# Optimization experiments

Measured on AMD Instinct MI355X. Metric: run time of the kernel, lower is better.

Reference implementation:

```python
import jax, jax.numpy as jnp
import numpy as np

B, H, N, L = 8, 128, 64, 8192
LOG_DT_MIN, LOG_DT_MAX = float(np.log(0.001)), float(np.log(0.1))


def setup_inputs() -> dict:
    key = jax.random.key(0)
    k_x, k_are, k_aim, k_c, k_dt = jax.random.split(key, 5)
    x = jax.random.normal(k_x, (B, H, L), dtype=jnp.float32)
    # A_re: negative real parts (clipped to <= -1e-4 in forward anyway)
    A_re = -jax.random.uniform(k_are, (H, N, 1), dtype=jnp.float32, minval=0.1, maxval=1.0)
    A_im = jax.random.normal(k_aim, (H, N, 1), dtype=jnp.float32) * float(np.pi)
    C = (0.5 ** 0.5) * jax.random.normal(k_c, (H, N, 2), dtype=jnp.float32)
    D = jnp.ones((1, H, 1), dtype=jnp.float32)
    u = jax.random.uniform(k_dt, (H, 1, 1), dtype=jnp.float32)
    log_delta = u * (LOG_DT_MAX - LOG_DT_MIN) + LOG_DT_MIN
    return {"x": x, "A_re": A_re, "A_im": A_im, "C": C, "D": D, "log_delta": log_delta}


def reference(x, A_re, A_im, C, D, log_delta):
    seq_len = x.shape[-1]
    # ---- S4D-ZOH kernel generation ----
    A = jnp.minimum(A_re, -1e-4) + 1j * A_im            # (H, N, 1) complex
    Cc = C[..., 0:1] + 1j * C[..., 1:2]                 # (H, N, 1) complex
    step = jnp.exp(log_delta)                           # (H, 1, 1)
    dA = step * A                                       # (H, N, 1)
    times = jnp.arange(seq_len, dtype=jnp.float32)[None, None, :]  # (1, 1, L)
    part = jnp.exp(times * dA)                          # (H, N, L)
    cons = (jnp.exp(dA) - 1.0) / A                      # (H, N, 1)
    K = jnp.sum(Cc * cons * part, axis=-2).real         # (H, L)
    # ---- causal conv via FFT (torch pads both to length 2L) ----
    n = seq_len + K.shape[-1]                           # 2L
    xd = jnp.fft.rfft(x, n=n, axis=-1)                  # (B, H, L+1)
    Kd = jnp.fft.rfft(K[None], n=n, axis=-1)            # (1, H, L+1)
    conv = jnp.fft.irfft(xd * Kd, n=n, axis=-1)[:, :, :seq_len]
    return conv + D * x
```

## Files before the change

kernel.cpp:

```cpp
#include <hip/hip_runtime.h>
#include <hip/hip_bf16.h>
#include <math.h>

#define B_ 8
#define H_ 128
#define N_ 64
#define L_ 8192
#define MCH 64
#define SCH (L_ / MCH)
#define EROW 136

typedef __attribute__((ext_vector_type(8))) short bf16x8;
typedef __attribute__((ext_vector_type(4))) float f32x4;

__device__ __forceinline__ float bf2f(ushort s) { return __uint_as_float(((uint)s) << 16); }
__device__ __forceinline__ uint packbf2(float a, float b) {
    __hip_bfloat162 h = __float22bfloat162_rn(make_float2(a, b));
    union { __hip_bfloat162 h2; uint u; } cv; cv.h2 = h;
    return cv.u;
}
__device__ __forceinline__ bf16x8 pack_bf8(float4 a, float4 b) {
    union { uint u[4]; bf16x8 v; } r;
    r.u[0] = packbf2(a.x, a.y); r.u[1] = packbf2(a.z, a.w);
    r.u[2] = packbf2(b.x, b.y); r.u[3] = packbf2(b.z, b.w);
    return r.v;
}

__global__ __launch_bounds__(256) void s4d_build(
    const float* __restrict__ A_re, const float* __restrict__ A_im,
    const float* __restrict__ C, const float* __restrict__ D,
    const float* __restrict__ log_delta,
    ushort* __restrict__ wsT, ushort* __restrict__ wsP,
    ushort* __restrict__ wsQ, float2* __restrict__ wsRM)
{
    __shared__ float kpart[64][65];
    __shared__ float kv[64];
    __shared__ uint  pbuf[64 * 68];

    const int h = blockIdx.x;
    const int tid = threadIdx.x;
    const int n = tid & 63;
    const int g = tid >> 6;

    float are = fminf(A_re[h * N_ + n], -1e-4f);
    float aim = A_im[h * N_ + n];
    float step = expf(log_delta[h]);
    float dre = step * are, dim = step * aim;
    float er = expf(dre);
    float sd, cd; sincosf(dim, &sd, &cd);
    float rr = er * cd;
    float ri = er * sd;
    float cre = C[(h * N_ + n) * 2 + 0];
    float cim = C[(h * N_ + n) * 2 + 1];
    float inv  = 1.0f / (are * are + aim * aim);
    float numr = rr - 1.0f, numi = ri;
    float consr = (numr * are + numi * aim) * inv;
    float consi = (numi * are - numr * aim) * inv;
    float wr = cre * consr - cim * consi;
    float wi = cre * consi + cim * consr;
    float dval = D[h];

    auto rp = [&](float d, float& pr, float& pi) {
        float e = __expf(d * dre);
        float ang = d * dim;
        float s = __sinf(ang), c2 = __cosf(ang);
        pr = e * c2; pi = e * s;
    };

#pragma unroll
    for (int j = 0; j < 16; ++j) {
        int d = g * 16 + j;
        float pr, pi; rp((float)d, pr, pi);
        kpart[d][n] = wr * pr - wi * pi;
    }
    __syncthreads();
    if (tid < 64) {
        float s = 0.f;
#pragma unroll
        for (int m = 0; m < 64; ++m) s += kpart[tid][m];
        kv[tid] = s;
    }
    __syncthreads();

    {
        uint tw[8];
#pragma unroll
        for (int i = 0; i < 8; ++i) {
            int t0 = g * 16 + 2 * i, t1 = t0 + 1;
            float v0 = (t0 <= n) ? kv[n - t0] : 0.f;
            float v1 = (t1 <= n) ? kv[n - t1] : 0.f;
            if (t0 == n) v0 += dval;
            if (t1 == n) v1 += dval;
            tw[i] = packbf2(v0, v1);
        }
        uint4* dT = (uint4*)(wsT + ((size_t)h * 64 + n) * 64 + g * 16);
        dT[0] = ((uint4*)tw)[0]; dT[1] = ((uint4*)tw)[1];
    }

    {
        uint qr[8], qi[8];
#pragma unroll
        for (int i = 0; i < 8; ++i) {
            int t0 = g * 16 + 2 * i;
            float ar0, ai0, ar1, ai1;
            rp((float)(63 - t0), ar0, ai0);
            rp((float)(62 - t0), ar1, ai1);
            qr[i] = packbf2(ar0, ar1);
            qi[i] = packbf2(ai0, ai1);
        }
        uint4* dQ0 = (uint4*)(wsQ + ((size_t)h * 128 + 2 * n    ) * 64 + g * 16);
        uint4* dQ1 = (uint4*)(wsQ + ((size_t)h * 128 + 2 * n + 1) * 64 + g * 16);
        dQ0[0] = ((uint4*)qr)[0]; dQ0[1] = ((uint4*)qr)[1];
        dQ1[0] = ((uint4*)qi)[0]; dQ1[1] = ((uint4*)qi)[1];
    }

#pragma unroll
    for (int i = 0; i < 16; ++i) {
        int j = g * 16 + i;
        float pr, pi; rp((float)(j + 1), pr, pi);
        float ur = wr * pr - wi * pi;
        float ui = wr * pi + wi * pr;
        pbuf[j * 68 + n] = packbf2(ur, -ui);
    }
    if (tid < 64) {
        float mr = rr, mi = ri;
#pragma unroll
        for (int k = 0; k < 6; ++k) { float tr = mr*mr - mi*mi, ti = 2.f*mr*mi; mr = tr; mi = ti; }
        wsRM[h * 64 + n] = make_float2(mr, mi);
    }
    __syncthreads();
    {
        uint4* dP = (uint4*)(wsP + ((size_t)h * 64 + n) * 128 + g * 32);
        const uint* src = &pbuf[n * 68 + g * 16];
        dP[0] = *(const uint4*)(src);
        dP[1] = *(const uint4*)(src + 4);
        dP[2] = *(const uint4*)(src + 8);
        dP[3] = *(const uint4*)(src + 12);
    }
}

__global__ __launch_bounds__(256, 4) void s4d_main(
    const float* __restrict__ x,
    const ushort* __restrict__ wsT, const ushort* __restrict__ wsP,
    const ushort* __restrict__ wsQ, const float2* __restrict__ wsRM,
    float* __restrict__ out)
{
    __shared__ ushort EBUF[SCH * EROW];
    __shared__ float segr[4][64], segi[4][64];

    const int seq = blockIdx.x;
    const int h   = seq % H_;
    const int tid = threadIdx.x;
    const int w   = tid >> 6;
    const int lane = tid & 63;
    const int n16 = lane & 15, q = lane >> 4;

    const float* xs = x + (size_t)seq * L_;

    bf16x8 xb[2][2];
#pragma unroll
    for (int ic = 0; ic < 2; ++ic) {
        int c = (2 * w + ic) * 16 + n16;
#pragma unroll
        for (int kc = 0; kc < 2; ++kc) {
            const float* p = xs + c * MCH + kc * 32 + q * 8;
            float4 f0 = *(const float4*)p;
            float4 f1 = *(const float4*)(p + 4);
            xb[ic][kc] = pack_bf8(f0, f1);
        }
    }

    const ushort* Qh = wsQ + (size_t)h * 128 * 64;
#pragma unroll
    for (int rt = 0; rt < 8; ++rt) {
        bf16x8 a0 = *(const bf16x8*)(Qh + ((size_t)(rt * 16 + n16)) * 64 +      q * 8);
        bf16x8 a1 = *(const bf16x8*)(Qh + ((size_t)(rt * 16 + n16)) * 64 + 32 + q * 8);
#pragma unroll
        for (int ic = 0; ic < 2; ++ic) {
            f32x4 acc = {0.f, 0.f, 0.f, 0.f};
            acc = __builtin_amdgcn_mfma_f32_16x16x32_bf16(a0, xb[ic][0], acc, 0, 0, 0);
            acc = __builtin_amdgcn_mfma_f32_16x16x32_bf16(a1, xb[ic][1], acc, 0, 0, 0);
            int c = (2 * w + ic) * 16 + n16;
            uint2 st = make_uint2(packbf2(acc[0], acc[1]), packbf2(acc[2], acc[3]));
            *(uint2*)&EBUF[c * EROW + rt * 16 + q * 4] = st;
        }
    }
    __syncthreads();

    {
        const int nB = tid & 63, gB = tid >> 6;
        float2 rm = wsRM[h * 64 + nB];
        float mr = rm.x, mi = rm.y;
        float m32r = mr, m32i = mi;
#pragma unroll
        for (int k = 0; k < 5; ++k) {
            float tr = m32r * m32r - m32i * m32i, ti = 2.f * m32r * m32i;
            m32r = tr; m32i = ti;
        }
        float sr = 0.f, si = 0.f;
#pragma unroll
        for (int j = 0; j < 32; ++j) {
            uint e = *(const uint*)&EBUF[(gB * 32 + j) * EROW + 2 * nB];
            float er2 = bf2f((ushort)(e & 0xffffu)), ei2 = bf2f((ushort)(e >> 16));
            float nr = er2 + mr * sr - mi * si;
            float ni = ei2 + mr * si + mi * sr;
            sr = nr; si = ni;
        }
        segr[gB][nB] = sr; segi[gB][nB] = si;
        __syncthreads();
        float pr2 = 0.f, pi2 = 0.f;
        for (int gp = 0; gp < gB; ++gp) {
            float Er = segr[gp][nB], Ei = segi[gp][nB];
            float nr = Er + m32r * pr2 - m32i * pi2;
            float ni = Ei + m32r * pi2 + m32i * pr2;
            pr2 = nr; pi2 = ni;
        }
        sr = pr2; si = pi2;
#pragma unroll
        for (int j = 0; j < 32; ++j) {
            uint* ep = (uint*)&EBUF[(gB * 32 + j) * EROW + 2 * nB];
            uint e = *ep;
            float er2 = bf2f((ushort)(e & 0xffffu)), ei2 = bf2f((ushort)(e >> 16));
            *ep = packbf2(sr, si);
            float nr = er2 + mr * sr - mi * si;
            float ni = ei2 + mr * si + mi * sr;
            sr = nr; si = ni;
        }
    }
    __syncthreads();

    const ushort* Th = wsT + (size_t)h * 64 * 64;
    const ushort* Ph = wsP + (size_t)h * 64 * 128;
    float* op = out + (size_t)seq * L_;
#pragma unroll
    for (int rt = 0; rt < 4; ++rt) {
        bf16x8 t0 = *(const bf16x8*)(Th + ((size_t)(rt * 16 + n16)) * 64 +      q * 8);
        bf16x8 t1 = *(const bf16x8*)(Th + ((size_t)(rt * 16 + n16)) * 64 + 32 + q * 8);
        bf16x8 p0 = *(const bf16x8*)(Ph + ((size_t)(rt * 16 + n16)) * 128 +       q * 8);
        bf16x8 p1 = *(const bf16x8*)(Ph + ((size_t)(rt * 16 + n16)) * 128 +  32 + q * 8);
        bf16x8 p2 = *(const bf16x8*)(Ph + ((size_t)(rt * 16 + n16)) * 128 +  64 + q * 8);
        bf16x8 p3 = *(const bf16x8*)(Ph + ((size_t)(rt * 16 + n16)) * 128 +  96 + q * 8);
#pragma unroll
        for (int ic = 0; ic < 2; ++ic) {
            int c = (2 * w + ic) * 16 + n16;
            f32x4 accT = {0.f, 0.f, 0.f, 0.f};
            f32x4 accP = {0.f, 0.f, 0.f, 0.f};
            accT = __builtin_amdgcn_mfma_f32_16x16x32_bf16(t0, xb[ic][0], accT, 0, 0, 0);
            accP = __builtin_amdgcn_mfma_f32_16x16x32_bf16(p0,
                       *(const bf16x8*)&EBUF[c * EROW +       q * 8], accP, 0, 0, 0);
            accT = __builtin_amdgcn_mfma_f32_16x16x32_bf16(t1, xb[ic][1], accT, 0, 0, 0);
            accP = __builtin_amdgcn_mfma_f32_16x16x32_bf16(p1,
                       *(const bf16x8*)&EBUF[c * EROW +  32 + q * 8], accP, 0, 0, 0);
            accP = __builtin_amdgcn_mfma_f32_16x16x32_bf16(p2,
                       *(const bf16x8*)&EBUF[c * EROW +  64 + q * 8], accP, 0, 0, 0);
            accP = __builtin_amdgcn_mfma_f32_16x16x32_bf16(p3,
                       *(const bf16x8*)&EBUF[c * EROW +  96 + q * 8], accP, 0, 0, 0);
            float4 o = make_float4(accT[0] + accP[0], accT[1] + accP[1],
                                   accT[2] + accP[2], accT[3] + accP[3]);
            *(float4*)(op + c * MCH + rt * 16 + q * 4) = o;
        }
    }
}

extern "C" void kernel_launch(void* const* d_in, const int* in_sizes, int n_in,
                              void* d_out, int out_size, void* d_ws, size_t ws_size,
                              hipStream_t stream)
{
    const float* x  = (const float*)d_in[0];
    const float* Ar = (const float*)d_in[1];
    const float* Ai = (const float*)d_in[2];
    const float* C  = (const float*)d_in[3];
    const float* D  = (const float*)d_in[4];
    const float* ld = (const float*)d_in[5];
    float* out = (float*)d_out;

    ushort* wsT = (ushort*)d_ws;
    ushort* wsP = wsT + (size_t)128 * 64 * 64;
    ushort* wsQ = wsP + (size_t)128 * 64 * 128;
    float2* wsRM = (float2*)(wsQ + (size_t)128 * 128 * 64);

    hipLaunchKernelGGL(s4d_build, dim3(H_), dim3(256), 0, stream,
                       Ar, Ai, C, D, ld, wsT, wsP, wsQ, wsRM);
    hipLaunchKernelGGL(s4d_main, dim3(B_ * H_), dim3(256), 0, stream,
                       x, wsT, wsP, wsQ, wsRM, out);
}
```

Baseline: 113.4 us.

## Split build kernel across two blocks per head and hoist T-matmul before scan

The build kernel now launches two blocks per head, each producing half of the T, Q and P tables, which doubles the parallelism of the small setup kernel. In the main kernel, the local Toeplitz MFMAs now run before the scan barrier and the first P tile is prefetched before the final sync, so matrix work and loads overlap with the scan. x is read and out is written with nontemporal loads and stores. In exchange, each thread holds the T accumulators in registers across the scan, which raises register pressure, and both build blocks redo the K reduction.

```diff
diff --git a/kernel.cpp b/kernel.cpp
--- a/kernel.cpp
+++ b/kernel.cpp
@@ -19,10 +19,10 @@
     union { __hip_bfloat162 h2; uint u; } cv; cv.h2 = h;
     return cv.u;
 }
-__device__ __forceinline__ bf16x8 pack_bf8(float4 a, float4 b) {
+__device__ __forceinline__ bf16x8 pack_bf8(f32x4 a, f32x4 b) {
     union { uint u[4]; bf16x8 v; } r;
-    r.u[0] = packbf2(a.x, a.y); r.u[1] = packbf2(a.z, a.w);
-    r.u[2] = packbf2(b.x, b.y); r.u[3] = packbf2(b.z, b.w);
+    r.u[0] = packbf2(a[0], a[1]); r.u[1] = packbf2(a[2], a[3]);
+    r.u[2] = packbf2(b[0], b[1]); r.u[3] = packbf2(b[2], b[3]);
     return r.v;
 }
 
@@ -35,9 +35,10 @@
 {
     __shared__ float kpart[64][65];
     __shared__ float kv[64];
-    __shared__ uint  pbuf[64 * 68];
-
-    const int h = blockIdx.x;
+    __shared__ uint  pbuf[32 * 68];
+
+    const int h = blockIdx.x >> 1;
+    const int e = blockIdx.x & 1;
     const int tid = threadIdx.x;
     const int n = tid & 63;
     const int g = tid >> 6;
@@ -48,12 +49,12 @@
     float dre = step * are, dim = step * aim;
     float er = expf(dre);
     float sd, cd; sincosf(dim, &sd, &cd);
-    float rr = er * cd;
-    float ri = er * sd;
+    float rre = er * cd;
+    float rim = er * sd;
     float cre = C[(h * N_ + n) * 2 + 0];
     float cim = C[(h * N_ + n) * 2 + 1];
     float inv  = 1.0f / (are * are + aim * aim);
-    float numr = rr - 1.0f, numi = ri;
+    float numr = rre - 1.0f, numi = rim;
     float consr = (numr * are + numi * aim) * inv;
     float consi = (numi * are - numr * aim) * inv;
     float wr = cre * consr - cim * consi;
@@ -61,10 +62,10 @@
     float dval = D[h];
 
     auto rp = [&](float d, float& pr, float& pi) {
-        float e = __expf(d * dre);
+        float ex = __expf(d * dre);
         float ang = d * dim;
         float s = __sinf(ang), c2 = __cosf(ang);
-        pr = e * c2; pi = e * s;
+        pr = ex * c2; pi = ex * s;
     };
 
 #pragma unroll
@@ -83,59 +84,56 @@
     __syncthreads();
 
     {
-        uint tw[8];
-#pragma unroll
-        for (int i = 0; i < 8; ++i) {
-            int t0 = g * 16 + 2 * i, t1 = t0 + 1;
+        uint tw[4];
+#pragma unroll
+        for (int i = 0; i < 4; ++i) {
+            int t0 = e * 32 + g * 8 + 2 * i, t1 = t0 + 1;
             float v0 = (t0 <= n) ? kv[n - t0] : 0.f;
             float v1 = (t1 <= n) ? kv[n - t1] : 0.f;
             if (t0 == n) v0 += dval;
             if (t1 == n) v1 += dval;
             tw[i] = packbf2(v0, v1);
         }
-        uint4* dT = (uint4*)(wsT + ((size_t)h * 64 + n) * 64 + g * 16);
-        dT[0] = ((uint4*)tw)[0]; dT[1] = ((uint4*)tw)[1];
+        *(uint4*)(wsT + ((size_t)h * 64 + n) * 64 + e * 32 + g * 8) = *(uint4*)tw;
     }
 
     {
-        uint qr[8], qi[8];
-#pragma unroll
-        for (int i = 0; i < 8; ++i) {
-            int t0 = g * 16 + 2 * i;
+        uint qr[4], qi[4];
+#pragma unroll
+        for (int i = 0; i < 4; ++i) {
+            int t0 = e * 32 + g * 8 + 2 * i;
             float ar0, ai0, ar1, ai1;
             rp((float)(63 - t0), ar0, ai0);
             rp((float)(62 - t0), ar1, ai1);
             qr[i] = packbf2(ar0, ar1);
             qi[i] = packbf2(ai0, ai1);
         }
-        uint4* dQ0 = (uint4*)(wsQ + ((size_t)h * 128 + 2 * n    ) * 64 + g * 16);
-        uint4* dQ1 = (uint4*)(wsQ + ((size_t)h * 128 + 2 * n + 1) * 64 + g * 16);
-        dQ0[0] = ((uint4*)qr)[0]; dQ0[1] = ((uint4*)qr)[1];
-        dQ1[0] = ((uint4*)qi)[0]; dQ1[1] = ((uint4*)qi)[1];
-    }
-
-#pragma unroll
-    for (int i = 0; i < 16; ++i) {
-        int j = g * 16 + i;
+        *(uint4*)(wsQ + ((size_t)h * 128 + 2 * n    ) * 64 + e * 32 + g * 8) = *(uint4*)qr;
+        *(uint4*)(wsQ + ((size_t)h * 128 + 2 * n + 1) * 64 + e * 32 + g * 8) = *(uint4*)qi;
+    }
+
+#pragma unroll
+    for (int i = 0; i < 8; ++i) {
+        int jl = g * 8 + i;
+        int j = e * 32 + jl;
         float pr, pi; rp((float)(j + 1), pr, pi);
         float ur = wr * pr - wi * pi;
         float ui = wr * pi + wi * pr;
-        pbuf[j * 68 + n] = packbf2(ur, -ui);
+        pbuf[jl * 68 + n] = packbf2(ur, -ui);
     }
     if (tid < 64) {
-        float mr = rr, mi = ri;
+        float mr = rre, mi = rim;
 #pragma unroll
         for (int k = 0; k < 6; ++k) { float tr = mr*mr - mi*mi, ti = 2.f*mr*mi; mr = tr; mi = ti; }
         wsRM[h * 64 + n] = make_float2(mr, mi);
     }
     __syncthreads();
     {
-        uint4* dP = (uint4*)(wsP + ((size_t)h * 64 + n) * 128 + g * 32);
-        const uint* src = &pbuf[n * 68 + g * 16];
+        const int rw = tid & 31, cc = tid >> 5;
+        const uint* src = &pbuf[rw * 68 + cc * 8];
+        uint4* dP = (uint4*)(wsP + ((size_t)h * 64 + e * 32 + rw) * 128 + cc * 16);
         dP[0] = *(const uint4*)(src);
         dP[1] = *(const uint4*)(src + 4);
-        dP[2] = *(const uint4*)(src + 8);
-        dP[3] = *(const uint4*)(src + 12);
     }
 }
 
@@ -164,8 +162,8 @@
 #pragma unroll
         for (int kc = 0; kc < 2; ++kc) {
             const float* p = xs + c * MCH + kc * 32 + q * 8;
-            float4 f0 = *(const float4*)p;
-            float4 f1 = *(const float4*)(p + 4);
+            f32x4 f0 = __builtin_nontemporal_load((const f32x4*)p);
+            f32x4 f1 = __builtin_nontemporal_load((const f32x4*)p + 1);
             xb[ic][kc] = pack_bf8(f0, f1);
         }
     }
@@ -183,6 +181,21 @@
             int c = (2 * w + ic) * 16 + n16;
             uint2 st = make_uint2(packbf2(acc[0], acc[1]), packbf2(acc[2], acc[3]));
             *(uint2*)&EBUF[c * EROW + rt * 16 + q * 4] = st;
+        }
+    }
+
+    const ushort* Th = wsT + (size_t)h * 64 * 64;
+    f32x4 accT[4][2];
+#pragma unroll
+    for (int rt = 0; rt < 4; ++rt) {
+        bf16x8 t0 = *(const bf16x8*)(Th + ((size_t)(rt * 16 + n16)) * 64 +      q * 8);
+        bf16x8 t1 = *(const bf16x8*)(Th + ((size_t)(rt * 16 + n16)) * 64 + 32 + q * 8);
+#pragma unroll
+        for (int ic = 0; ic < 2; ++ic) {
+            f32x4 a = {0.f, 0.f, 0.f, 0.f};
+            a = __builtin_amdgcn_mfma_f32_16x16x32_bf16(t0, xb[ic][0], a, 0, 0, 0);
+            a = __builtin_amdgcn_mfma_f32_16x16x32_bf16(t1, xb[ic][1], a, 0, 0, 0);
+            accT[rt][ic] = a;
         }
     }
     __syncthreads();
@@ -227,37 +240,43 @@
             sr = nr; si = ni;
         }
     }
-    __syncthreads();
-
-    const ushort* Th = wsT + (size_t)h * 64 * 64;
+
     const ushort* Ph = wsP + (size_t)h * 64 * 128;
+    bf16x8 pf0 = *(const bf16x8*)(Ph + (size_t)n16 * 128 +       q * 8);
+    bf16x8 pf1 = *(const bf16x8*)(Ph + (size_t)n16 * 128 +  32 + q * 8);
+    bf16x8 pf2 = *(const bf16x8*)(Ph + (size_t)n16 * 128 +  64 + q * 8);
+    bf16x8 pf3 = *(const bf16x8*)(Ph + (size_t)n16 * 128 +  96 + q * 8);
+    __syncthreads();
+
     float* op = out + (size_t)seq * L_;
 #pragma unroll
     for (int rt = 0; rt < 4; ++rt) {
-        bf16x8 t0 = *(const bf16x8*)(Th + ((size_t)(rt * 16 + n16)) * 64 +      q * 8);
-        bf16x8 t1 = *(const bf16x8*)(Th + ((size_t)(rt * 16 + n16)) * 64 + 32 + q * 8);
-        bf16x8 p0 = *(const bf16x8*)(Ph + ((size_t)(rt * 16 + n16)) * 128 +       q * 8);
-        bf16x8 p1 = *(const bf16x8*)(Ph + ((size_t)(rt * 16 + n16)) * 128 +  32 + q * 8);
-        bf16x8 p2 = *(const bf16x8*)(Ph + ((size_t)(rt * 16 + n16)) * 128 +  64 + q * 8);
-        bf16x8 p3 = *(const bf16x8*)(Ph + ((size_t)(rt * 16 + n16)) * 128 +  96 + q * 8);
+        bf16x8 p0, p1, p2, p3;
+        if (rt == 0) { p0 = pf0; p1 = pf1; p2 = pf2; p3 = pf3; }
+        else {
+            p0 = *(const bf16x8*)(Ph + ((size_t)(rt * 16 + n16)) * 128 +       q * 8);
+            p1 = *(const bf16x8*)(Ph + ((size_t)(rt * 16 + n16)) * 128 +  32 + q * 8);
+            p2 = *(const bf16x8*)(Ph + ((size_t)(rt * 16 + n16)) * 128 +  64 + q * 8);
+            p3 = *(const bf16x8*)(Ph + ((size_t)(rt * 16 + n16)) * 128 +  96 + q * 8);
+        }
 #pragma unroll
         for (int ic = 0; ic < 2; ++ic) {
             int c = (2 * w + ic) * 16 + n16;
-            f32x4 accT = {0.f, 0.f, 0.f, 0.f};
             f32x4 accP = {0.f, 0.f, 0.f, 0.f};
-            accT = __builtin_amdgcn_mfma_f32_16x16x32_bf16(t0, xb[ic][0], accT, 0, 0, 0);
             accP = __builtin_amdgcn_mfma_f32_16x16x32_bf16(p0,
                        *(const bf16x8*)&EBUF[c * EROW +       q * 8], accP, 0, 0, 0);
-            accT = __builtin_amdgcn_mfma_f32_16x16x32_bf16(t1, xb[ic][1], accT, 0, 0, 0);
             accP = __builtin_amdgcn_mfma_f32_16x16x32_bf16(p1,
                        *(const bf16x8*)&EBUF[c * EROW +  32 + q * 8], accP, 0, 0, 0);
             accP = __builtin_amdgcn_mfma_f32_16x16x32_bf16(p2,
                        *(const bf16x8*)&EBUF[c * EROW +  64 + q * 8], accP, 0, 0, 0);
             accP = __builtin_amdgcn_mfma_f32_16x16x32_bf16(p3,
                        *(const bf16x8*)&EBUF[c * EROW +  96 + q * 8], accP, 0, 0, 0);
-            float4 o = make_float4(accT[0] + accP[0], accT[1] + accP[1],
-                                   accT[2] + accP[2], accT[3] + accP[3]);
-            *(float4*)(op + c * MCH + rt * 16 + q * 4) = o;
+            f32x4 o;
+            o[0] = accT[rt][ic][0] + accP[0];
+            o[1] = accT[rt][ic][1] + accP[1];
+            o[2] = accT[rt][ic][2] + accP[2];
+            o[3] = accT[rt][ic][3] + accP[3];
+            __builtin_nontemporal_store(o, (f32x4*)(op + c * MCH + rt * 16 + q * 4));
         }
     }
 }
@@ -279,7 +298,7 @@
     ushort* wsQ = wsP + (size_t)128 * 64 * 128;
     float2* wsRM = (float2*)(wsQ + (size_t)128 * 128 * 64);
 
-    hipLaunchKernelGGL(s4d_build, dim3(H_), dim3(256), 0, stream,
+    hipLaunchKernelGGL(s4d_build, dim3(H_ * 2), dim3(256), 0, stream,
                        Ar, Ai, C, D, ld, wsT, wsP, wsQ, wsRM);
     hipLaunchKernelGGL(s4d_main, dim3(B_ * H_), dim3(256), 0, stream,
                        x, wsT, wsP, wsQ, wsRM, out);
```

Result: no change. 115.4 us (+1.8%).
